# Kernel tuning notes

Measured on AMD Instinct MI355X. Metric: run time of the kernel, lower is better.

The kernel has to match this reference:

```python
import jax, jax.numpy as jnp
from jax import lax
import numpy as np

B, C, H, W, OUTC, KS = 4, 64, 128, 128, 64, 3
N = KS * KS
PAD = 1
STRIDE = 1


def conv2d(x, w, b, stride, pad):
    out = lax.conv_general_dilated(x, w, (stride, stride), ((pad, pad), (pad, pad)),
                                   dimension_numbers=('NCHW', 'OIHW', 'NCHW'))
    if b is not None:
        out = out + b[None, :, None, None]
    return out


def setup_inputs() -> dict:
    key = jax.random.key(0)
    k = jax.random.split(key, 8)
    f = jnp.float32

    def w_init(kk, shape, fan_in, scale=1.0):
        return jax.random.normal(kk, shape, f) * (scale / np.sqrt(fan_in))

    return {
        'x': jax.random.normal(k[0], (B, C, H, W), f),
        'ref': jax.random.normal(k[1], (B, C, H, W), f),
        'w_cd': w_init(k[2], (C, 2 * C, 1, 1), 2 * C),
        'b_cd': jnp.zeros((C,), f),
        'w_p': w_init(k[3], (2 * N, C, 3, 3), C * 9, 0.1),  # small offsets, keeps sampling stable
        'b_p': jnp.zeros((2 * N,), f),
        'w_m': w_init(k[4], (N, C, 3, 3), C * 9),
        'b_m': jnp.zeros((N,), f),
        'w_c': w_init(k[5], (N * C, C, 3, 3), C * 9),
        'b_c': jnp.zeros((N * C,), f),
        'w_conv': w_init(k[6], (OUTC, C, KS, KS), C * KS * KS),
    }


def deform_forward(x, ref, w_cd, b_cd, w_p, b_p, w_m, b_m, w_c, b_c, w_conv):
    b, c, h, w = x.shape
    fused = conv2d(jnp.concatenate([x, ref], axis=1), w_cd, b_cd, 1, 0)
    offset = conv2d(fused, w_p, b_p, STRIDE, 1)             # [b, 2N, h, w]
    m = jax.nn.sigmoid(conv2d(fused, w_m, b_m, STRIDE, 1))  # [b, N, h, w]
    c_off = jnp.tanh(conv2d(fused, w_c, b_c, STRIDE, 1))    # [b, N*c, h, w]

    xp = jnp.pad(x, ((0, 0), (0, 0), (PAD, PAD), (PAD, PAD)))
    Hp, Wp = h + 2 * PAD, w + 2 * PAD

    # kernel-relative grid p_n (first N entries = rows, last N = cols)
    r = jnp.arange(-(KS - 1) // 2, (KS - 1) // 2 + 1)
    pnx, pny = jnp.meshgrid(r, r, indexing='ij')
    p_n = jnp.concatenate([pnx.ravel(), pny.ravel()]).reshape(1, 2 * N, 1, 1)
    # base grid p_0 starts at 1 because of the zero padding
    gx, gy = jnp.meshgrid(jnp.arange(1, h * STRIDE + 1, STRIDE),
                          jnp.arange(1, w * STRIDE + 1, STRIDE), indexing='ij')
    p_0 = jnp.concatenate([jnp.broadcast_to(gx[None, None], (1, N, h, w)),
                           jnp.broadcast_to(gy[None, None], (1, N, h, w))], axis=1)
    p = (p_0 + p_n).astype(offset.dtype) + offset           # [b, 2N, h, w]
    p = p.transpose(0, 2, 3, 1)                             # [b, h, w, 2N]

    q_lt = jnp.floor(lax.stop_gradient(p))
    q_rb = q_lt + 1

    def clampq(q):
        return jnp.concatenate([jnp.clip(q[..., :N], 0, Hp - 1),
                                jnp.clip(q[..., N:], 0, Wp - 1)], axis=-1).astype(jnp.int32)

    q_lt = clampq(q_lt)
    q_rb = clampq(q_rb)
    q_lb = jnp.concatenate([q_lt[..., :N], q_rb[..., N:]], axis=-1)
    q_rt = jnp.concatenate([q_rb[..., :N], q_lt[..., N:]], axis=-1)
    p = jnp.concatenate([jnp.clip(p[..., :N], 0, Hp - 1),
                         jnp.clip(p[..., N:], 0, Wp - 1)], axis=-1)

    def gweight(q, sx, sy):
        qx = q[..., :N].astype(p.dtype)
        qy = q[..., N:].astype(p.dtype)
        return (1 + sx * (qx - p[..., :N])) * (1 + sy * (qy - p[..., N:]))

    g_lt = gweight(q_lt, 1, 1)
    g_rb = gweight(q_rb, -1, -1)
    g_lb = gweight(q_lb, 1, -1)
    g_rt = gweight(q_rt, -1, 1)

    x_flat = xp.reshape(b, c, Hp * Wp)

    def get_x_q(q):
        idx = q[..., :N] * Wp + q[..., N:]                  # [b, h, w, N]
        xq = jnp.take_along_axis(x_flat, idx.reshape(b, 1, -1), axis=2)
        return xq.reshape(b, c, h, w, N)

    x_off = (g_lt[:, None] * get_x_q(q_lt) + g_rb[:, None] * get_x_q(q_rb)
             + g_lb[:, None] * get_x_q(q_lb) + g_rt[:, None] * get_x_q(q_rt))

    # color deformation: [b, N*c, h, w] -> [b, c, h, w, N]
    x_off = x_off + c_off.reshape(b, c, N, h, w).transpose(0, 1, 3, 4, 2)
    # modulation broadcast over channels
    x_off = x_off * m.transpose(0, 2, 3, 1)[:, None]

    # [b,c,h,w,N] -> [b,c,h*ks,w*ks] with N = (kernel_row, kernel_col)
    x_off = x_off.reshape(b, c, h, w, KS, KS).transpose(0, 1, 2, 4, 3, 5)
    x_off = x_off.reshape(b, c, h * KS, w * KS)
    return conv2d(x_off, w_conv, None, KS, 0)


def reference(x, ref, w_cd, b_cd, w_p, b_p, w_m, b_m, w_c, b_c, w_conv):
    return deform_forward(x, ref, w_cd, b_cd, w_p, b_p, w_m, b_m, w_c, b_c, w_conv)
```

## Files before the change

kernel.cpp:

```cpp
#include <hip/hip_runtime.h>
#include <hip/hip_fp16.h>


typedef __attribute__((ext_vector_type(8))) __bf16 bf16x8;
typedef __attribute__((ext_vector_type(16))) float f32x16;
#define MFMA32(a, b, c) __builtin_amdgcn_mfma_f32_32x32x16_bf16((a), (b), (c), 0, 0, 0)

#define WS_AC    0
#define WS_APM   368640
#define WS_ACONV 387072
#define WS_WCD   428032
#define WS_F2    436224

struct f2pair { float x, y; };

__device__ __forceinline__ unsigned short f2bf(float f) {
    unsigned u = __float_as_uint(f);
    return (unsigned short)((u + 0x7FFFu + ((u >> 16) & 1u)) >> 16);
}
__device__ __forceinline__ float fast_rcp(float x) {
#if __has_builtin(__builtin_amdgcn_rcpf)
    return __builtin_amdgcn_rcpf(x);
#else
    return 1.0f / x;
#endif
}
__device__ __forceinline__ float fast_tanh(float x) {
    float t = __expf(2.0f * x);
    return 1.0f - 2.0f * fast_rcp(t + 1.0f);
}
__device__ __forceinline__ float fast_sigmoid(float x) {
    return fast_rcp(1.0f + __expf(-x));
}

__global__ void prep_kernel(const float* __restrict__ w_c, const float* __restrict__ w_p,
                            const float* __restrict__ w_m, const float* __restrict__ w_conv,
                            const float* __restrict__ w_cd, unsigned short* __restrict__ ws) {
    int i = blockIdx.x * 256 + threadIdx.x;
    if (i >= 436224) return;
    float val;
    if (i < WS_APM) {
        int t = i, j = t & 7, l = (t >> 3) & 63, r = t >> 9, ks = r % 36, gmt = r / 36;
        int row = gmt * 32 + (l & 31);
        int kp = ks * 16 + (l >> 5) * 8 + j, tap = kp >> 6, ci = kp & 63;
        val = (row < 576) ? w_c[row * 576 + ci * 9 + tap] : 0.0f;
    } else if (i < WS_ACONV) {
        int t = i - WS_APM, j = t & 7, l = (t >> 3) & 63, ks = t >> 9;
        int row = l & 31;
        int kp = ks * 16 + (l >> 5) * 8 + j, tap = kp >> 6, ci = kp & 63;
        val = (row < 18) ? w_p[row * 576 + ci * 9 + tap]
            : (row < 27) ? w_m[(row - 18) * 576 + ci * 9 + tap] : 0.0f;
    } else if (i < WS_WCD) {
        int t = i - WS_ACONV, j = t & 7, l = (t >> 3) & 63, r = t >> 9;
        int gks = r % 40, ocT = r / 40;
        int oc = ocT * 32 + (l & 31);
        int krow = gks * 16 + (l >> 5) * 8 + j;
        val = (krow < 576) ? w_conv[oc * 576 + krow] : 0.0f;
    } else {
        val = w_cd[i - WS_WCD];
    }
    ws[i] = f2bf(val);
}

__device__ __forceinline__ uint4 stage_load64(const unsigned short* f2b, int h,
                                              int px0, int chunk, int tid) {
    int tap = chunk >> 1;
    int dh = tap / 3 - 1, dw = tap % 3 - 1;
    int hs = h + dh;
    int kg = tid >> 6, px = tid & 63;
    int cg = (chunk & 1) * 4 + kg;
    int wsrc = px0 + px + dw;
    uint4 pk = {0u, 0u, 0u, 0u};
    if (((unsigned)hs < 128u) && ((unsigned)wsrc < 128u))
        pk = *(const uint4*)(f2b + (((size_t)cg << 14) + (hs << 7) + wsrc) * 8);
    return pk;
}
__device__ __forceinline__ void stage_write64(char* Bst, uint4 pk, int tid) {
    int kg = tid >> 6, px = tid & 63;
    *(uint4*)(Bst + ((kg >> 1) * 2 + (px >> 5)) * 1024
                  + ((px & 31) + 32 * (kg & 1)) * 16) = pk;
}

__global__ __launch_bounds__(256, 4)
void k2_fused(const float* __restrict__ x, const float* __restrict__ ref,
              const float* __restrict__ b_cd, const unsigned short* __restrict__ wsbf,
              unsigned short* __restrict__ ws) {
    __shared__ __align__(16) char B0[32768];
    const int tid = threadIdx.x, l = tid & 63, w = tid >> 6;
    const int b = blockIdx.y, p0 = blockIdx.x * 128;
    const int rl31 = l & 31, kh8 = (l >> 5) * 8;

    #pragma unroll
    for (int it = 0; it < 8; ++it) {
        int task = it * 256 + tid;
        int kg = task >> 7, px = task & 127;
        const float* src = (kg < 8) ? x : ref;
        int kbase = (kg & 7) * 8;
        unsigned short v[8];
        #pragma unroll
        for (int j = 0; j < 8; ++j)
            v[j] = f2bf(src[(((size_t)b * 64 + kbase + j) << 14) + p0 + px]);
        uint4 pk;
        pk.x = (unsigned)v[0] | ((unsigned)v[1] << 16);
        pk.y = (unsigned)v[2] | ((unsigned)v[3] << 16);
        pk.z = (unsigned)v[4] | ((unsigned)v[5] << 16);
        pk.w = (unsigned)v[6] | ((unsigned)v[7] << 16);
        *(uint4*)(B0 + ((kg >> 1) * 4 + (px >> 5)) * 1024
                      + ((px & 31) + 32 * (kg & 1)) * 16) = pk;
    }
    __syncthreads();

    f32x16 a0, a1;
    #pragma unroll
    for (int r = 0; r < 16; ++r) { a0[r] = 0.0f; a1[r] = 0.0f; }
    const unsigned short* A0 = wsbf + WS_WCD + rl31 * 128 + kh8;
    #pragma unroll
    for (int s = 0; s < 8; ++s) {
        bf16x8 bf = *(bf16x8*)(B0 + ((s * 4 + w) * 64 + l) * 16);
        bf16x8 x0 = *(const bf16x8*)(A0 + s * 16);
        bf16x8 x1 = *(const bf16x8*)(A0 + 32 * 128 + s * 16);
        a0 = MFMA32(x0, bf, a0);
        a1 = MFMA32(x1, bf, a1);
    }
    unsigned short* f2 = ws + WS_F2 + ((size_t)b << 20);
    int px = p0 + w * 32 + rl31;
    int h4 = (l >> 5) * 4;
    #pragma unroll
    for (int t = 0; t < 2; ++t)
        #pragma unroll
        for (int q = 0; q < 4; ++q) {
            ushort4 st;
            float v0 = (t ? a1[q * 4 + 0] : a0[q * 4 + 0]) + b_cd[t * 32 + 8 * q + h4 + 0];
            float v1 = (t ? a1[q * 4 + 1] : a0[q * 4 + 1]) + b_cd[t * 32 + 8 * q + h4 + 1];
            float v2 = (t ? a1[q * 4 + 2] : a0[q * 4 + 2]) + b_cd[t * 32 + 8 * q + h4 + 2];
            float v3 = (t ? a1[q * 4 + 3] : a0[q * 4 + 3]) + b_cd[t * 32 + 8 * q + h4 + 3];
            st.x = f2bf(v0); st.y = f2bf(v1); st.z = f2bf(v2); st.w = f2bf(v3);
            *(ushort4*)(f2 + ((size_t)((t * 4 + q) << 14) + px) * 8 + h4) = st;
        }
}

__global__ __launch_bounds__(256, 4)
void k3_main(const float* __restrict__ x, const float* __restrict__ b_c,
             const float* __restrict__ b_p, const float* __restrict__ b_m,
             const unsigned short* __restrict__ wsbf, float* __restrict__ out) {
    __shared__ __align__(16) char lds[36096];
    char* Bst0 = lds;
    char* Bst1 = lds + 4096;
    char* Amod = lds + 8192;
    float* uL = (float*)(lds + 8192);
    short* sidx = (short*)(lds + 24576);
    unsigned short* w4h = (unsigned short*)(lds + 26880);
    float* mL = (float*)(lds + 31488);
    float* bcL = (float*)(lds + 33792);

    const int tid = threadIdx.x, l = tid & 63, w = tid >> 6;
    const int id = blockIdx.x;
    const int hbLin = (id & 7) * 128 + (id >> 3);
    const int half = hbLin & 1, b = (hbLin >> 1) & 3, h = hbLin >> 3;
    const int px0 = half * 64;
    const unsigned short* f2b = wsbf + WS_F2 + ((size_t)b << 20);

    for (int i = tid; i < 576; i += 256) bcL[i] = b_c[i];

    {
        f32x16 pm;
        #pragma unroll
        for (int r = 0; r < 16; ++r) pm[r] = 0.0f;
        stage_write64(Bst0, stage_load64(f2b, h, px0, 0, tid), tid);
        __syncthreads();
        #pragma unroll 1
        for (int it = 0; it < 18; ++it) {
            char* cur = (it & 1) ? Bst1 : Bst0;
            char* nxt = (it & 1) ? Bst0 : Bst1;
            uint4 pk;
            if (it < 17) pk = stage_load64(f2b, h, px0, it + 1, tid);
            if (w < 2) {
                #pragma unroll
                for (int s = 0; s < 2; ++s) {
                    int ks = it * 2 + s;
                    bf16x8 bf = *(bf16x8*)(cur + ((s * 2 + w) * 64 + l) * 16);
                    bf16x8 apm = *(const bf16x8*)(wsbf + WS_APM + ((ks * 64 + l) << 3));
                    pm = MFMA32(apm, bf, pm);
                }
            }
            if (it < 17) stage_write64(nxt, pk, tid);
            __syncthreads();
        }
        if (w < 2) {
            int pxp = w * 32 + (l & 31);
            #pragma unroll
            for (int reg = 0; reg < 16; ++reg) {
                int rl = (reg & 3) + 8 * (reg >> 2) + 4 * (l >> 5);
                uL[rl * 64 + pxp] = pm[reg];
            }
        }
        __syncthreads();
    }

    #pragma unroll 1
    for (int i = tid; i < 576; i += 256) {
        int n = i >> 6, px = i & 63;
        float offr = uL[n * 64 + px] + b_p[n];
        float offc = uL[(9 + n) * 64 + px] + b_p[9 + n];
        float mraw = uL[(18 + n) * 64 + px] + b_m[n];
        int nr = n / 3, nc = n - nr * 3;
        float pr = (float)(h + nr) + offr;
        float pc = (float)(px0 + px + nc) + offc;
        float flr = floorf(pr), flc = floorf(pc);
        float prc = fminf(fmaxf(pr, 0.0f), 129.0f);
        float pcc = fminf(fmaxf(pc, 0.0f), 129.0f);
        float q0r = fminf(fmaxf(flr, 0.0f), 129.0f);
        float q1r = fminf(fmaxf(flr + 1.0f, 0.0f), 129.0f);
        int ir0 = (int)q0r, ir1 = (int)q1r;
        bool vr0 = (ir0 >= 1) && (ir0 <= 128), vr1 = (ir1 >= 1) && (ir1 <= 128);
        float wr0 = vr0 ? (1.0f + q0r - prc) : 0.0f;
        float wr1 = vr1 ? (1.0f - (q1r - prc)) : 0.0f;
        float q0c = fminf(fmaxf(flc, 0.0f), 129.0f);
        float q1c = fminf(fmaxf(flc + 1.0f, 0.0f), 129.0f);
        int ic0 = (int)q0c, ic1 = (int)q1c;
        bool vc0 = (ic0 >= 1) && (ic0 <= 128), vc1 = (ic1 >= 1) && (ic1 <= 128);
        float wc0 = vc0 ? (1.0f + q0c - pcc) : 0.0f;
        float wc1 = vc1 ? (1.0f - (q1c - pcc)) : 0.0f;
        int cx0 = ic0 - 1, cx1 = ic1 - 1;
        int base = min(max(cx0, 0), 126);
        float ws0 = ((base == cx0) && vc0 ? wc0 : 0.0f)
                  + ((base == cx1) && vc1 ? wc1 : 0.0f);
        float ws1 = ((base + 1 == cx0) && vc0 ? wc0 : 0.0f)
                  + ((base + 1 == cx1) && vc1 ? wc1 : 0.0f);
        int rx0 = min(max(ir0 - 1, 0), 127), rx1 = min(max(ir1 - 1, 0), 127);
        short2 s2;
        s2.x = (short)(rx0 * 128 + base);
        s2.y = (short)(rx1 * 128 + base);
        ((short2*)sidx)[px * 9 + n] = s2;
        int wb = (px * 9 + n) * 4;
        w4h[wb + 0] = __half_as_ushort(__float2half(wr0 * ws0));
        w4h[wb + 1] = __half_as_ushort(__float2half(wr0 * ws1));
        w4h[wb + 2] = __half_as_ushort(__float2half(wr1 * ws0));
        w4h[wb + 3] = __half_as_ushort(__float2half(wr1 * ws1));
        mL[n * 64 + px] = fast_sigmoid(mraw);
    }
    __syncthreads();

    f32x16 oa;
    #pragma unroll
    for (int r = 0; r < 16; ++r) oa[r] = 0.0f;
    const float* xb = x + (((size_t)b * 64) << 14);
    const int ocT = w >> 1, nT2 = w & 1;

    #pragma unroll 1
    for (int p = 0; p < 5; ++p) {
        const int mt = p * 4 + w;
        f32x16 acc[2];
        #pragma unroll
        for (int j = 0; j < 2; ++j)
            #pragma unroll
            for (int r = 0; r < 16; ++r) acc[j][r] = 0.0f;

        stage_write64(Bst0, stage_load64(f2b, h, px0, 0, tid), tid);
        __syncthreads();
        #pragma unroll 1
        for (int it = 0; it < 18; ++it) {
            char* cur = (it & 1) ? Bst1 : Bst0;
            char* nxt = (it & 1) ? Bst0 : Bst1;
            uint4 pk;
            if (it < 17) pk = stage_load64(f2b, h, px0, it + 1, tid);
            #pragma unroll
            for (int s = 0; s < 2; ++s) {
                const int ks = it * 2 + s;
                bf16x8 bf0 = *(bf16x8*)(cur + ((s * 2 + 0) * 64 + l) * 16);
                bf16x8 bf1 = *(bf16x8*)(cur + ((s * 2 + 1) * 64 + l) * 16);
                bf16x8 af = *(const bf16x8*)(wsbf + WS_AC
                                + (((mt * 36 + ks) * 64 + l) << 3));
                acc[0] = MFMA32(af, bf0, acc[0]);
                acc[1] = MFMA32(af, bf1, acc[1]);
            }
            if (it < 17) stage_write64(nxt, pk, tid);
            __syncthreads();
        }

        const int rowbase = mt * 32;
        #pragma unroll
        for (int j = 0; j < 2; ++j) {
            const int pxe = j * 32 + (l & 31);
            if (rowbase < 576) {
                #pragma unroll
                for (int reg = 0; reg < 16; ++reg) {
                    int rl = (reg & 3) + 8 * (reg >> 2) + 4 * (l >> 5);
                    int row = rowbase + rl;
                    int c = row / 9, n = row - c * 9;
                    float uv = acc[j][reg] + bcL[row];
                    float t = fast_tanh(uv);
                    short2 s2 = ((short2*)sidx)[pxe * 9 + n];
                    int wb = (pxe * 9 + n) * 4;
                    float w0 = __half2float(__ushort_as_half(w4h[wb + 0]));
                    float w1 = __half2float(__ushort_as_half(w4h[wb + 1]));
                    float w2 = __half2float(__ushort_as_half(w4h[wb + 2]));
                    float w3 = __half2float(__ushort_as_half(w4h[wb + 3]));
                    const float* xp = xb + ((size_t)c << 14);
                    f2pair v0 = *(const f2pair*)(xp + s2.x);
                    f2pair v1 = *(const f2pair*)(xp + s2.y);
                    float samp = w0 * v0.x + w1 * v0.y + w2 * v1.x + w3 * v1.y;
                    acc[j][reg] = mL[n * 64 + pxe] * (samp + t);
                    if ((reg & 3) == 3) __builtin_amdgcn_sched_barrier(0);
                }
            } else {
                #pragma unroll
                for (int reg = 0; reg < 16; ++reg) acc[j][reg] = 0.0f;
            }
        }

        __syncthreads();
        #pragma unroll
        for (int j = 0; j < 2; ++j) {
            #pragma unroll
            for (int reg = 0; reg < 16; ++reg) {
                int rl = (reg & 3) + 8 * (reg >> 2) + 4 * (l >> 5);
                int k = w * 32 + rl;
                *(unsigned short*)(Amod + ((k >> 4) * 2 + j) * 1024
                        + ((l & 31) + 32 * ((k >> 3) & 1)) * 16 + (k & 7) * 2)
                    = f2bf(acc[j][reg]);
            }
        }
        __syncthreads();
        #pragma unroll
        for (int ks8 = 0; ks8 < 8; ++ks8) {
            bf16x8 af = *(const bf16x8*)(wsbf + WS_ACONV
                            + (((ocT * 40 + p * 8 + ks8) * 64 + l) << 3));
            bf16x8 bf = *(bf16x8*)(Amod + (ks8 * 2 + nT2) * 1024 + l * 16);
            oa = MFMA32(af, bf, oa);
        }
    }

    float* ob = out + (((size_t)b * 64) << 14) + (h << 7) + px0 + nT2 * 32 + (l & 31);
    #pragma unroll
    for (int reg = 0; reg < 16; ++reg) {
        int rl = (reg & 3) + 8 * (reg >> 2) + 4 * (l >> 5);
        int oc = ocT * 32 + rl;
        ob[(size_t)oc << 14] = oa[reg];
    }
}

extern "C" void kernel_launch(void* const* d_in, const int* in_sizes, int n_in,
                              void* d_out, int out_size, void* d_ws, size_t ws_size,
                              hipStream_t stream) {
    const float* x      = (const float*)d_in[0];
    const float* ref    = (const float*)d_in[1];
    const float* w_cd   = (const float*)d_in[2];
    const float* b_cd   = (const float*)d_in[3];
    const float* w_p    = (const float*)d_in[4];
    const float* b_p    = (const float*)d_in[5];
    const float* w_m    = (const float*)d_in[6];
    const float* b_m    = (const float*)d_in[7];
    const float* w_c    = (const float*)d_in[8];
    const float* b_c    = (const float*)d_in[9];
    const float* w_conv = (const float*)d_in[10];
    float* out = (float*)d_out;
    unsigned short* wsbf = (unsigned short*)d_ws;

    hipLaunchKernelGGL(prep_kernel, dim3(1704), dim3(256), 0, stream,
                       w_c, w_p, w_m, w_conv, w_cd, wsbf);
    hipLaunchKernelGGL(k2_fused, dim3(128, 4), dim3(256), 0, stream,
                       x, ref, b_cd, wsbf, wsbf);
    hipLaunchKernelGGL(k3_main, dim3(1024), dim3(256), 0, stream,
                       x, b_c, b_p, b_m, wsbf, out);
}
```

Measured before the change: 223.9 us.

## Double K-step staging depth and alias LDS regions to halve barriers

The staging loops now process two 64-wide K slices per iteration with 8KB double buffers and prefetch two slices ahead in registers, so each loop runs 9 iterations and synchronises half as often. All LDS regions (staging, uL, Amod) are aliased onto one buffer, which shrinks the LDS footprint and may raise occupancy. The four half-precision weight loads are merged into a single 8-byte LDS read. Barrier placement is reworked to cover the aliasing, which raises the risk of races between the index-setup stage and the next staging writes.

```diff
diff --git a/kernel.cpp b/kernel.cpp
--- a/kernel.cpp
+++ b/kernel.cpp
@@ -143,15 +143,13 @@
 void k3_main(const float* __restrict__ x, const float* __restrict__ b_c,
              const float* __restrict__ b_p, const float* __restrict__ b_m,
              const unsigned short* __restrict__ wsbf, float* __restrict__ out) {
-    __shared__ __align__(16) char lds[36096];
-    char* Bst0 = lds;
-    char* Bst1 = lds + 4096;
-    char* Amod = lds + 8192;
-    float* uL = (float*)(lds + 8192);
-    short* sidx = (short*)(lds + 24576);
-    unsigned short* w4h = (unsigned short*)(lds + 26880);
-    float* mL = (float*)(lds + 31488);
-    float* bcL = (float*)(lds + 33792);
+    __shared__ __align__(16) char lds[27904];
+    char* R = lds;
+    float* uL = (float*)lds;
+    short* sidx = (short*)(lds + 16384);
+    unsigned short* w4h = (unsigned short*)(lds + 18688);
+    float* mL = (float*)(lds + 23296);
+    float* bcL = (float*)(lds + 25600);
 
     const int tid = threadIdx.x, l = tid & 63, w = tid >> 6;
     const int id = blockIdx.x;
@@ -166,25 +164,38 @@
         f32x16 pm;
         #pragma unroll
         for (int r = 0; r < 16; ++r) pm[r] = 0.0f;
-        stage_write64(Bst0, stage_load64(f2b, h, px0, 0, tid), tid);
+        uint4 a0 = stage_load64(f2b, h, px0, 0, tid);
+        uint4 a1 = stage_load64(f2b, h, px0, 1, tid);
+        stage_write64(R, a0, tid);
+        stage_write64(R + 4096, a1, tid);
+        uint4 b0 = stage_load64(f2b, h, px0, 2, tid);
+        uint4 b1 = stage_load64(f2b, h, px0, 3, tid);
         __syncthreads();
         #pragma unroll 1
-        for (int it = 0; it < 18; ++it) {
-            char* cur = (it & 1) ? Bst1 : Bst0;
-            char* nxt = (it & 1) ? Bst0 : Bst1;
-            uint4 pk;
-            if (it < 17) pk = stage_load64(f2b, h, px0, it + 1, tid);
+        for (int it = 0; it < 9; ++it) {
+            char* cur = R + (it & 1) * 8192;
+            char* nxt = R + ((it + 1) & 1) * 8192;
+            uint4 c0 = b0, c1 = b1;
+            if (it < 7) {
+                c0 = stage_load64(f2b, h, px0, 2 * it + 4, tid);
+                c1 = stage_load64(f2b, h, px0, 2 * it + 5, tid);
+            }
             if (w < 2) {
                 #pragma unroll
-                for (int s = 0; s < 2; ++s) {
-                    int ks = it * 2 + s;
-                    bf16x8 bf = *(bf16x8*)(cur + ((s * 2 + w) * 64 + l) * 16);
+                for (int q = 0; q < 4; ++q) {
+                    int ks = it * 4 + q;
+                    bf16x8 bf = *(bf16x8*)(cur + (q >> 1) * 4096
+                                               + (((q & 1) * 2 + w) * 64 + l) * 16);
                     bf16x8 apm = *(const bf16x8*)(wsbf + WS_APM + ((ks * 64 + l) << 3));
                     pm = MFMA32(apm, bf, pm);
                 }
             }
-            if (it < 17) stage_write64(nxt, pk, tid);
+            if (it < 8) {
+                stage_write64(nxt, b0, tid);
+                stage_write64(nxt + 4096, b1, tid);
+            }
             __syncthreads();
+            b0 = c0; b1 = c1;
         }
         if (w < 2) {
             int pxp = w * 32 + (l & 31);
@@ -239,7 +250,6 @@
         w4h[wb + 3] = __half_as_ushort(__float2half(wr1 * ws1));
         mL[n * 64 + px] = fast_sigmoid(mraw);
     }
-    __syncthreads();
 
     f32x16 oa;
     #pragma unroll
@@ -256,26 +266,41 @@
             #pragma unroll
             for (int r = 0; r < 16; ++r) acc[j][r] = 0.0f;
 
-        stage_write64(Bst0, stage_load64(f2b, h, px0, 0, tid), tid);
-        __syncthreads();
+        uint4 a0 = stage_load64(f2b, h, px0, 0, tid);
+        uint4 a1 = stage_load64(f2b, h, px0, 1, tid);
+        uint4 b0 = stage_load64(f2b, h, px0, 2, tid);
+        uint4 b1 = stage_load64(f2b, h, px0, 3, tid);
+        __syncthreads();
+        stage_write64(R, a0, tid);
+        stage_write64(R + 4096, a1, tid);
+        __syncthreads();
+
         #pragma unroll 1
-        for (int it = 0; it < 18; ++it) {
-            char* cur = (it & 1) ? Bst1 : Bst0;
-            char* nxt = (it & 1) ? Bst0 : Bst1;
-            uint4 pk;
-            if (it < 17) pk = stage_load64(f2b, h, px0, it + 1, tid);
+        for (int it = 0; it < 9; ++it) {
+            char* cur = R + (it & 1) * 8192;
+            char* nxt = R + ((it + 1) & 1) * 8192;
+            uint4 c0 = b0, c1 = b1;
+            if (it < 7) {
+                c0 = stage_load64(f2b, h, px0, 2 * it + 4, tid);
+                c1 = stage_load64(f2b, h, px0, 2 * it + 5, tid);
+            }
             #pragma unroll
-            for (int s = 0; s < 2; ++s) {
-                const int ks = it * 2 + s;
-                bf16x8 bf0 = *(bf16x8*)(cur + ((s * 2 + 0) * 64 + l) * 16);
-                bf16x8 bf1 = *(bf16x8*)(cur + ((s * 2 + 1) * 64 + l) * 16);
+            for (int q = 0; q < 4; ++q) {
+                const int ks = it * 4 + q;
+                char* fb = cur + (q >> 1) * 4096;
+                bf16x8 bf0 = *(bf16x8*)(fb + (((q & 1) * 2 + 0) * 64 + l) * 16);
+                bf16x8 bf1 = *(bf16x8*)(fb + (((q & 1) * 2 + 1) * 64 + l) * 16);
                 bf16x8 af = *(const bf16x8*)(wsbf + WS_AC
                                 + (((mt * 36 + ks) * 64 + l) << 3));
                 acc[0] = MFMA32(af, bf0, acc[0]);
                 acc[1] = MFMA32(af, bf1, acc[1]);
             }
-            if (it < 17) stage_write64(nxt, pk, tid);
+            if (it < 8) {
+                stage_write64(nxt, b0, tid);
+                stage_write64(nxt + 4096, b1, tid);
+            }
             __syncthreads();
+            b0 = c0; b1 = c1;
         }
 
         const int rowbase = mt * 32;
@@ -292,10 +317,11 @@
                     float t = fast_tanh(uv);
                     short2 s2 = ((short2*)sidx)[pxe * 9 + n];
                     int wb = (pxe * 9 + n) * 4;
-                    float w0 = __half2float(__ushort_as_half(w4h[wb + 0]));
-                    float w1 = __half2float(__ushort_as_half(w4h[wb + 1]));
-                    float w2 = __half2float(__ushort_as_half(w4h[wb + 2]));
-                    float w3 = __half2float(__ushort_as_half(w4h[wb + 3]));
+                    uint2 wv = *(const uint2*)(w4h + wb);
+                    float w0 = __half2float(__ushort_as_half((unsigned short)(wv.x & 0xffffu)));
+                    float w1 = __half2float(__ushort_as_half((unsigned short)(wv.x >> 16)));
+                    float w2 = __half2float(__ushort_as_half((unsigned short)(wv.y & 0xffffu)));
+                    float w3 = __half2float(__ushort_as_half((unsigned short)(wv.y >> 16)));
                     const float* xp = xb + ((size_t)c << 14);
                     f2pair v0 = *(const f2pair*)(xp + s2.x);
                     f2pair v1 = *(const f2pair*)(xp + s2.y);
@@ -309,14 +335,13 @@
             }
         }
 
-        __syncthreads();
         #pragma unroll
         for (int j = 0; j < 2; ++j) {
             #pragma unroll
             for (int reg = 0; reg < 16; ++reg) {
                 int rl = (reg & 3) + 8 * (reg >> 2) + 4 * (l >> 5);
                 int k = w * 32 + rl;
-                *(unsigned short*)(Amod + ((k >> 4) * 2 + j) * 1024
+                *(unsigned short*)(R + ((k >> 4) * 2 + j) * 1024
                         + ((l & 31) + 32 * ((k >> 3) & 1)) * 16 + (k & 7) * 2)
                     = f2bf(acc[j][reg]);
             }
@@ -326,7 +351,7 @@
         for (int ks8 = 0; ks8 < 8; ++ks8) {
             bf16x8 af = *(const bf16x8*)(wsbf + WS_ACONV
                             + (((ocT * 40 + p * 8 + ks8) * 64 + l) << 3));
-            bf16x8 bf = *(bf16x8*)(Amod + (ks8 * 2 + nT2) * 1024 + l * 16);
+            bf16x8 bf = *(bf16x8*)(R + (ks8 * 2 + nT2) * 1024 + l * 16);
             oa = MFMA32(af, bf, oa);
         }
     }
```

Measured after the change: 224.5 us. Within noise of the previous version (+0.3%).

## Fuse weight prep into k2 and merge offset GEMM with first channel-offset pass

Applied to the files above, without the earlier changes.

Removes the separate weight-conversion kernel: k2 now converts the w_c/w_p/w_m/w_conv weights to bf16 with a grid-stride loop and loads w_cd into shared memory, saving one launch. In k3 the offset/mask GEMM is fused with the first pass of the colour-offset GEMM, so the staged f2 tiles are loaded once less and all four waves do MFMA work during the offset phase. The per-pixel sampling table is packed into one 16-byte record per pixel and tap, so each lookup is a single LDS load. In exchange, k2 does extra conversion work with more LDS, and k3 holds an extra accumulator, which adds register pressure.

```diff
diff --git a/kernel.cpp b/kernel.cpp
--- a/kernel.cpp
+++ b/kernel.cpp
@@ -9,7 +9,6 @@
 #define WS_AC    0
 #define WS_APM   368640
 #define WS_ACONV 387072
-#define WS_WCD   428032
 #define WS_F2    436224
 
 struct f2pair { float x, y; };
@@ -31,35 +30,6 @@
 }
 __device__ __forceinline__ float fast_sigmoid(float x) {
     return fast_rcp(1.0f + __expf(-x));
-}
-
-__global__ void prep_kernel(const float* __restrict__ w_c, const float* __restrict__ w_p,
-                            const float* __restrict__ w_m, const float* __restrict__ w_conv,
-                            const float* __restrict__ w_cd, unsigned short* __restrict__ ws) {
-    int i = blockIdx.x * 256 + threadIdx.x;
-    if (i >= 436224) return;
-    float val;
-    if (i < WS_APM) {
-        int t = i, j = t & 7, l = (t >> 3) & 63, r = t >> 9, ks = r % 36, gmt = r / 36;
-        int row = gmt * 32 + (l & 31);
-        int kp = ks * 16 + (l >> 5) * 8 + j, tap = kp >> 6, ci = kp & 63;
-        val = (row < 576) ? w_c[row * 576 + ci * 9 + tap] : 0.0f;
-    } else if (i < WS_ACONV) {
-        int t = i - WS_APM, j = t & 7, l = (t >> 3) & 63, ks = t >> 9;
-        int row = l & 31;
-        int kp = ks * 16 + (l >> 5) * 8 + j, tap = kp >> 6, ci = kp & 63;
-        val = (row < 18) ? w_p[row * 576 + ci * 9 + tap]
-            : (row < 27) ? w_m[(row - 18) * 576 + ci * 9 + tap] : 0.0f;
-    } else if (i < WS_WCD) {
-        int t = i - WS_ACONV, j = t & 7, l = (t >> 3) & 63, r = t >> 9;
-        int gks = r % 40, ocT = r / 40;
-        int oc = ocT * 32 + (l & 31);
-        int krow = gks * 16 + (l >> 5) * 8 + j;
-        val = (krow < 576) ? w_conv[oc * 576 + krow] : 0.0f;
-    } else {
-        val = w_cd[i - WS_WCD];
-    }
-    ws[i] = f2bf(val);
 }
 
 __device__ __forceinline__ uint4 stage_load64(const unsigned short* f2b, int h,
@@ -83,12 +53,45 @@
 
 __global__ __launch_bounds__(256, 4)
 void k2_fused(const float* __restrict__ x, const float* __restrict__ ref,
-              const float* __restrict__ b_cd, const unsigned short* __restrict__ wsbf,
+              const float* __restrict__ b_cd, const float* __restrict__ w_c,
+              const float* __restrict__ w_p, const float* __restrict__ w_m,
+              const float* __restrict__ w_conv, const float* __restrict__ w_cd,
               unsigned short* __restrict__ ws) {
     __shared__ __align__(16) char B0[32768];
+    __shared__ __align__(16) unsigned short WcdL[8192];
     const int tid = threadIdx.x, l = tid & 63, w = tid >> 6;
     const int b = blockIdx.y, p0 = blockIdx.x * 128;
     const int rl31 = l & 31, kh8 = (l >> 5) * 8;
+
+    {
+        int gtid = (blockIdx.y * 128 + blockIdx.x) * 256 + tid;
+        #pragma unroll 1
+        for (int i = gtid; i < 428032; i += 131072) {
+            float val;
+            if (i < WS_APM) {
+                int t = i, jj = t & 7, lx = (t >> 3) & 63, r = t >> 9;
+                int ks = r % 36, gmt = r / 36;
+                int row = gmt * 32 + (lx & 31);
+                int kp = ks * 16 + (lx >> 5) * 8 + jj, tap = kp >> 6, ci = kp & 63;
+                val = (row < 576) ? w_c[row * 576 + ci * 9 + tap] : 0.0f;
+            } else if (i < WS_ACONV) {
+                int t = i - WS_APM, jj = t & 7, lx = (t >> 3) & 63, ks = t >> 9;
+                int row = lx & 31;
+                int kp = ks * 16 + (lx >> 5) * 8 + jj, tap = kp >> 6, ci = kp & 63;
+                val = (row < 18) ? w_p[row * 576 + ci * 9 + tap]
+                    : (row < 27) ? w_m[(row - 18) * 576 + ci * 9 + tap] : 0.0f;
+            } else {
+                int t = i - WS_ACONV, jj = t & 7, lx = (t >> 3) & 63, r = t >> 9;
+                int gks = r % 40, ocT2 = r / 40;
+                int oc = ocT2 * 32 + (lx & 31);
+                int krow = gks * 16 + (lx >> 5) * 8 + jj;
+                val = (krow < 576) ? w_conv[oc * 576 + krow] : 0.0f;
+            }
+            ws[i] = f2bf(val);
+        }
+    }
+    #pragma unroll
+    for (int i = tid; i < 8192; i += 256) WcdL[i] = f2bf(w_cd[i]);
 
     #pragma unroll
     for (int it = 0; it < 8; ++it) {
@@ -113,7 +116,7 @@
     f32x16 a0, a1;
     #pragma unroll
     for (int r = 0; r < 16; ++r) { a0[r] = 0.0f; a1[r] = 0.0f; }
-    const unsigned short* A0 = wsbf + WS_WCD + rl31 * 128 + kh8;
+    const unsigned short* A0 = WcdL + rl31 * 128 + kh8;
     #pragma unroll
     for (int s = 0; s < 8; ++s) {
         bf16x8 bf = *(bf16x8*)(B0 + ((s * 4 + w) * 64 + l) * 16);
@@ -148,24 +151,68 @@
     char* Bst1 = lds + 4096;
     char* Amod = lds + 8192;
     float* uL = (float*)(lds + 8192);
-    short* sidx = (short*)(lds + 24576);
-    unsigned short* w4h = (unsigned short*)(lds + 26880);
-    float* mL = (float*)(lds + 31488);
+    char* tbl = lds + 24576;
     float* bcL = (float*)(lds + 33792);
 
     const int tid = threadIdx.x, l = tid & 63, w = tid >> 6;
+    const int lh = l >> 5, l31 = l & 31;
     const int id = blockIdx.x;
     const int hbLin = (id & 7) * 128 + (id >> 3);
     const int half = hbLin & 1, b = (hbLin >> 1) & 3, h = hbLin >> 3;
     const int px0 = half * 64;
     const unsigned short* f2b = wsbf + WS_F2 + ((size_t)b << 20);
+    const float* xb = x + (((size_t)b * 64) << 14);
+    const int ocT = w >> 1, nT2 = w & 1;
 
     for (int i = tid; i < 576; i += 256) bcL[i] = b_c[i];
 
+    f32x16 oa;
+
+    auto epi = [&](f32x16& a, int j, int rowbase) {
+        const int pxe = j * 32 + l31;
+        if (rowbase < 576) {
+            #pragma unroll
+            for (int reg = 0; reg < 16; ++reg) {
+                int rl = (reg & 3) + 8 * (reg >> 2) + 4 * lh;
+                int row = rowbase + rl;
+                int c = row / 9, n = row - c * 9;
+                float uv = a[reg] + bcL[row];
+                float t = fast_tanh(uv);
+                uint4 rec = *(const uint4*)(tbl + (pxe * 9 + n) * 16);
+                float w0 = __half2float(__ushort_as_half((unsigned short)(rec.x & 0xffffu)));
+                float w1 = __half2float(__ushort_as_half((unsigned short)(rec.x >> 16)));
+                float w2 = __half2float(__ushort_as_half((unsigned short)(rec.y & 0xffffu)));
+                float w3 = __half2float(__ushort_as_half((unsigned short)(rec.y >> 16)));
+                int i0 = (int)(rec.z & 0xffffu);
+                int i1 = (int)(rec.z >> 16);
+                float mval = __uint_as_float(rec.w);
+                const float* xp = xb + ((size_t)c << 14);
+                f2pair v0 = *(const f2pair*)(xp + i0);
+                f2pair v1 = *(const f2pair*)(xp + i1);
+                float samp = w0 * v0.x + w1 * v0.y + w2 * v1.x + w3 * v1.y;
+                a[reg] = mval * (samp + t);
+                if ((reg & 3) == 3) __builtin_amdgcn_sched_barrier(0);
+            }
+        } else {
+            #pragma unroll
+            for (int reg = 0; reg < 16; ++reg) a[reg] = 0.0f;
+        }
+    };
+    auto scat = [&](const f32x16& a, int j) {
+        #pragma unroll
+        for (int reg = 0; reg < 16; ++reg) {
+            int rl = (reg & 3) + 8 * (reg >> 2) + 4 * lh;
+            int k = w * 32 + rl;
+            *(unsigned short*)(Amod + ((k >> 4) * 2 + j) * 1024
+                    + (l31 + 32 * ((k >> 3) & 1)) * 16 + (k & 7) * 2)
+                = f2bf(a[reg]);
+        }
+    };
+
     {
-        f32x16 pm;
-        #pragma unroll
-        for (int r = 0; r < 16; ++r) pm[r] = 0.0f;
+        f32x16 acc0, acc1, pm;
+        #pragma unroll
+        for (int r = 0; r < 16; ++r) { acc0[r] = 0.0f; acc1[r] = 0.0f; pm[r] = 0.0f; }
         stage_write64(Bst0, stage_load64(f2b, h, px0, 0, tid), tid);
         __syncthreads();
         #pragma unroll 1
@@ -174,87 +221,98 @@
             char* nxt = (it & 1) ? Bst0 : Bst1;
             uint4 pk;
             if (it < 17) pk = stage_load64(f2b, h, px0, it + 1, tid);
-            if (w < 2) {
-                #pragma unroll
-                for (int s = 0; s < 2; ++s) {
-                    int ks = it * 2 + s;
-                    bf16x8 bf = *(bf16x8*)(cur + ((s * 2 + w) * 64 + l) * 16);
+            #pragma unroll
+            for (int s = 0; s < 2; ++s) {
+                const int ks = it * 2 + s;
+                bf16x8 bf0 = *(bf16x8*)(cur + ((s * 2 + 0) * 64 + l) * 16);
+                bf16x8 bf1 = *(bf16x8*)(cur + ((s * 2 + 1) * 64 + l) * 16);
+                bf16x8 af = *(const bf16x8*)(wsbf + WS_AC
+                                + (((w * 36 + ks) * 64 + l) << 3));
+                acc0 = MFMA32(af, bf0, acc0);
+                acc1 = MFMA32(af, bf1, acc1);
+                if (w < 2) {
                     bf16x8 apm = *(const bf16x8*)(wsbf + WS_APM + ((ks * 64 + l) << 3));
-                    pm = MFMA32(apm, bf, pm);
+                    pm = MFMA32(apm, w ? bf1 : bf0, pm);
                 }
             }
             if (it < 17) stage_write64(nxt, pk, tid);
             __syncthreads();
         }
         if (w < 2) {
-            int pxp = w * 32 + (l & 31);
+            int pxp = w * 32 + l31;
             #pragma unroll
             for (int reg = 0; reg < 16; ++reg) {
-                int rl = (reg & 3) + 8 * (reg >> 2) + 4 * (l >> 5);
+                int rl = (reg & 3) + 8 * (reg >> 2) + 4 * lh;
                 uL[rl * 64 + pxp] = pm[reg];
             }
         }
         __syncthreads();
+
+        #pragma unroll 1
+        for (int i = tid; i < 576; i += 256) {
+            int n = i >> 6, px = i & 63;
+            float offr = uL[n * 64 + px] + b_p[n];
+            float offc = uL[(9 + n) * 64 + px] + b_p[9 + n];
+            float mraw = uL[(18 + n) * 64 + px] + b_m[n];
+            int nr = n / 3, nc = n - nr * 3;
+            float pr = (float)(h + nr) + offr;
+            float pc = (float)(px0 + px + nc) + offc;
+            float flr = floorf(pr), flc = floorf(pc);
+            float prc = fminf(fmaxf(pr, 0.0f), 129.0f);
+            float pcc = fminf(fmaxf(pc, 0.0f), 129.0f);
+            float q0r = fminf(fmaxf(flr, 0.0f), 129.0f);
+            float q1r = fminf(fmaxf(flr + 1.0f, 0.0f), 129.0f);
+            int ir0 = (int)q0r, ir1 = (int)q1r;
+            bool vr0 = (ir0 >= 1) && (ir0 <= 128), vr1 = (ir1 >= 1) && (ir1 <= 128);
+            float wr0 = vr0 ? (1.0f + q0r - prc) : 0.0f;
+            float wr1 = vr1 ? (1.0f - (q1r - prc)) : 0.0f;
+            float q0c = fminf(fmaxf(flc, 0.0f), 129.0f);
+            float q1c = fminf(fmaxf(flc + 1.0f, 0.0f), 129.0f);
+            int ic0 = (int)q0c, ic1 = (int)q1c;
+            bool vc0 = (ic0 >= 1) && (ic0 <= 128), vc1 = (ic1 >= 1) && (ic1 <= 128);
+            float wc0 = vc0 ? (1.0f + q0c - pcc) : 0.0f;
+            float wc1 = vc1 ? (1.0f - (q1c - pcc)) : 0.0f;
+            int cx0 = ic0 - 1, cx1 = ic1 - 1;
+            int base = min(max(cx0, 0), 126);
+            float ws0 = ((base == cx0) && vc0 ? wc0 : 0.0f)
+                      + ((base == cx1) && vc1 ? wc1 : 0.0f);
+            float ws1 = ((base + 1 == cx0) && vc0 ? wc0 : 0.0f)
+                      + ((base + 1 == cx1) && vc1 ? wc1 : 0.0f);
+            int rx0 = min(max(ir0 - 1, 0), 127), rx1 = min(max(ir1 - 1, 0), 127);
+            uint4 rec;
+            rec.x = (unsigned)__half_as_ushort(__float2half(wr0 * ws0))
+                  | ((unsigned)__half_as_ushort(__float2half(wr0 * ws1)) << 16);
+            rec.y = (unsigned)__half_as_ushort(__float2half(wr1 * ws0))
+                  | ((unsigned)__half_as_ushort(__float2half(wr1 * ws1)) << 16);
+            rec.z = (unsigned)(unsigned short)(rx0 * 128 + base)
+                  | ((unsigned)(unsigned short)(rx1 * 128 + base) << 16);
+            rec.w = __float_as_uint(fast_sigmoid(mraw));
+            *(uint4*)(tbl + (px * 9 + n) * 16) = rec;
+        }
+        __syncthreads();
+
+        epi(acc0, 0, w * 32);
+        epi(acc1, 1, w * 32);
+        #pragma unroll
+        for (int r = 0; r < 16; ++r) oa[r] = 0.0f;
+        scat(acc0, 0);
+        scat(acc1, 1);
+        __syncthreads();
+        #pragma unroll
+        for (int ks8 = 0; ks8 < 8; ++ks8) {
+            bf16x8 af = *(const bf16x8*)(wsbf + WS_ACONV
+                            + (((ocT * 40 + ks8) * 64 + l) << 3));
+            bf16x8 bf = *(bf16x8*)(Amod + (ks8 * 2 + nT2) * 1024 + l * 16);
+            oa = MFMA32(af, bf, oa);
+        }
     }
 
     #pragma unroll 1
-    for (int i = tid; i < 576; i += 256) {
-        int n = i >> 6, px = i & 63;
-        float offr = uL[n * 64 + px] + b_p[n];
-        float offc = uL[(9 + n) * 64 + px] + b_p[9 + n];
-        float mraw = uL[(18 + n) * 64 + px] + b_m[n];
-        int nr = n / 3, nc = n - nr * 3;
-        float pr = (float)(h + nr) + offr;
-        float pc = (float)(px0 + px + nc) + offc;
-        float flr = floorf(pr), flc = floorf(pc);
-        float prc = fminf(fmaxf(pr, 0.0f), 129.0f);
-        float pcc = fminf(fmaxf(pc, 0.0f), 129.0f);
-        float q0r = fminf(fmaxf(flr, 0.0f), 129.0f);
-        float q1r = fminf(fmaxf(flr + 1.0f, 0.0f), 129.0f);
-        int ir0 = (int)q0r, ir1 = (int)q1r;
-        bool vr0 = (ir0 >= 1) && (ir0 <= 128), vr1 = (ir1 >= 1) && (ir1 <= 128);
-        float wr0 = vr0 ? (1.0f + q0r - prc) : 0.0f;
-        float wr1 = vr1 ? (1.0f - (q1r - prc)) : 0.0f;
-        float q0c = fminf(fmaxf(flc, 0.0f), 129.0f);
-        float q1c = fminf(fmaxf(flc + 1.0f, 0.0f), 129.0f);
-        int ic0 = (int)q0c, ic1 = (int)q1c;
-        bool vc0 = (ic0 >= 1) && (ic0 <= 128), vc1 = (ic1 >= 1) && (ic1 <= 128);
-        float wc0 = vc0 ? (1.0f + q0c - pcc) : 0.0f;
-        float wc1 = vc1 ? (1.0f - (q1c - pcc)) : 0.0f;
-        int cx0 = ic0 - 1, cx1 = ic1 - 1;
-        int base = min(max(cx0, 0), 126);
-        float ws0 = ((base == cx0) && vc0 ? wc0 : 0.0f)
-                  + ((base == cx1) && vc1 ? wc1 : 0.0f);
-        float ws1 = ((base + 1 == cx0) && vc0 ? wc0 : 0.0f)
-                  + ((base + 1 == cx1) && vc1 ? wc1 : 0.0f);
-        int rx0 = min(max(ir0 - 1, 0), 127), rx1 = min(max(ir1 - 1, 0), 127);
-        short2 s2;
-        s2.x = (short)(rx0 * 128 + base);
-        s2.y = (short)(rx1 * 128 + base);
-        ((short2*)sidx)[px * 9 + n] = s2;
-        int wb = (px * 9 + n) * 4;
-        w4h[wb + 0] = __half_as_ushort(__float2half(wr0 * ws0));
-        w4h[wb + 1] = __half_as_ushort(__float2half(wr0 * ws1));
-        w4h[wb + 2] = __half_as_ushort(__float2half(wr1 * ws0));
-        w4h[wb + 3] = __half_as_ushort(__float2half(wr1 * ws1));
-        mL[n * 64 + px] = fast_sigmoid(mraw);
-    }
-    __syncthreads();
-
-    f32x16 oa;
-    #pragma unroll
-    for (int r = 0; r < 16; ++r) oa[r] = 0.0f;
-    const float* xb = x + (((size_t)b * 64) << 14);
-    const int ocT = w >> 1, nT2 = w & 1;
-
-    #pragma unroll 1
-    for (int p = 0; p < 5; ++p) {
+    for (int p = 1; p < 5; ++p) {
         const int mt = p * 4 + w;
-        f32x16 acc[2];
-        #pragma unroll
-        for (int j = 0; j < 2; ++j)
-            #pragma unroll
-            for (int r = 0; r < 16; ++r) acc[j][r] = 0.0f;
+        f32x16 acc0, acc1;
+        #pragma unroll
+        for (int r = 0; r < 16; ++r) { acc0[r] = 0.0f; acc1[r] = 0.0f; }
 
         stage_write64(Bst0, stage_load64(f2b, h, px0, 0, tid), tid);
         __syncthreads();
@@ -271,56 +329,19 @@
                 bf16x8 bf1 = *(bf16x8*)(cur + ((s * 2 + 1) * 64 + l) * 16);
                 bf16x8 af = *(const bf16x8*)(wsbf + WS_AC
                                 + (((mt * 36 + ks) * 64 + l) << 3));
-                acc[0] = MFMA32(af, bf0, acc[0]);
-                acc[1] = MFMA32(af, bf1, acc[1]);
+                acc0 = MFMA32(af, bf0, acc0);
+                acc1 = MFMA32(af, bf1, acc1);
             }
             if (it < 17) stage_write64(nxt, pk, tid);
             __syncthreads();
         }
 
-        const int rowbase = mt * 32;
-        #pragma unroll
-        for (int j = 0; j < 2; ++j) {
-            const int pxe = j * 32 + (l & 31);
-            if (rowbase < 576) {
-                #pragma unroll
-                for (int reg = 0; reg < 16; ++reg) {
-                    int rl = (reg & 3) + 8 * (reg >> 2) + 4 * (l >> 5);
-                    int row = rowbase + rl;
-                    int c = row / 9, n = row - c * 9;
-                    float uv = acc[j][reg] + bcL[row];
-                    float t = fast_tanh(uv);
-                    short2 s2 = ((short2*)sidx)[pxe * 9 + n];
-                    int wb = (pxe * 9 + n) * 4;
-                    float w0 = __half2float(__ushort_as_half(w4h[wb + 0]));
-                    float w1 = __half2float(__ushort_as_half(w4h[wb + 1]));
-                    float w2 = __half2float(__ushort_as_half(w4h[wb + 2]));
-                    float w3 = __half2float(__ushort_as_half(w4h[wb + 3]));
-                    const float* xp = xb + ((size_t)c << 14);
-                    f2pair v0 = *(const f2pair*)(xp + s2.x);
-                    f2pair v1 = *(const f2pair*)(xp + s2.y);
-                    float samp = w0 * v0.x + w1 * v0.y + w2 * v1.x + w3 * v1.y;
-                    acc[j][reg] = mL[n * 64 + pxe] * (samp + t);
-                    if ((reg & 3) == 3) __builtin_amdgcn_sched_barrier(0);
-                }
-            } else {
-                #pragma unroll
-                for (int reg = 0; reg < 16; ++reg) acc[j][reg] = 0.0f;
-            }
-        }
-
-        __syncthreads();
-        #pragma unroll
-        for (int j = 0; j < 2; ++j) {
-            #pragma unroll
-            for (int reg = 0; reg < 16; ++reg) {
-                int rl = (reg & 3) + 8 * (reg >> 2) + 4 * (l >> 5);
-                int k = w * 32 + rl;
-                *(unsigned short*)(Amod + ((k >> 4) * 2 + j) * 1024
-                        + ((l & 31) + 32 * ((k >> 3) & 1)) * 16 + (k & 7) * 2)
-                    = f2bf(acc[j][reg]);
-            }
-        }
+        epi(acc0, 0, mt * 32);
+        epi(acc1, 1, mt * 32);
+
+        __syncthreads();
+        scat(acc0, 0);
+        scat(acc1, 1);
         __syncthreads();
         #pragma unroll
         for (int ks8 = 0; ks8 < 8; ++ks8) {
@@ -331,10 +352,10 @@
         }
     }
 
-    float* ob = out + (((size_t)b * 64) << 14) + (h << 7) + px0 + nT2 * 32 + (l & 31);
+    float* ob = out + (((size_t)b * 64) << 14) + (h << 7) + px0 + nT2 * 32 + l31;
     #pragma unroll
     for (int reg = 0; reg < 16; ++reg) {
-        int rl = (reg & 3) + 8 * (reg >> 2) + 4 * (l >> 5);
+        int rl = (reg & 3) + 8 * (reg >> 2) + 4 * lh;
         int oc = ocT * 32 + rl;
         ob[(size_t)oc << 14] = oa[reg];
     }
@@ -357,10 +378,8 @@
     float* out = (float*)d_out;
     unsigned short* wsbf = (unsigned short*)d_ws;
 
-    hipLaunchKernelGGL(prep_kernel, dim3(1704), dim3(256), 0, stream,
-                       w_c, w_p, w_m, w_conv, w_cd, wsbf);
     hipLaunchKernelGGL(k2_fused, dim3(128, 4), dim3(256), 0, stream,
-                       x, ref, b_cd, wsbf, wsbf);
+                       x, ref, b_cd, w_c, w_p, w_m, w_conv, w_cd, wsbf);
     hipLaunchKernelGGL(k3_main, dim3(1024), dim3(256), 0, stream,
                        x, b_c, b_p, b_m, wsbf, out);
 }
```

New measurement: 233.6 us. +4.4%, slower.
